# Optimization experiments

Measured on AMD Instinct MI355X. Metric: run time of the kernel, lower is better.

The kernel has to match this reference:

```python
import jax, jax.numpy as jnp
import numpy as np

H = 128          # hidden_channels
L = 2            # num_layers
E = 400000       # edges per relation
N_ATOM = 600000
N = (20000, 20000, 10000)  # node counts: 0=Chemical, 1=Gene, 2=Assay
OUT = 2          # out_channels
# (src_type, dst_type) per relation, matching the HeteroConv_att dict order
RELS = ((0,2),(0,2),(0,1),(0,1),(0,1),(2,1),(1,1),(2,0),(2,0),(1,0),(1,0),(1,0),(1,2))
R = len(RELS)
NEG_SLOPE = 0.2  # GATv2 LeakyReLU slope


def setup_inputs() -> dict:
    key = jax.random.key(0)
    ks = jax.random.split(key, 16)
    sc = 1.0 / np.sqrt(H)
    x_atom  = jax.random.normal(ks[0], (N_ATOM, H), jnp.float32)
    x_chem  = jax.random.normal(ks[1], (N[0], H), jnp.float32)
    x_gene  = jax.random.normal(ks[2], (N[1], H), jnp.float32)
    x_assay = jax.random.normal(ks[3], (N[2], H), jnp.float32)
    hyper_dst = jax.random.randint(ks[4], (N_ATOM,), 0, N[0], jnp.int32)
    ei = []
    for r, (s, d) in enumerate(RELS):
        src = jax.random.randint(jax.random.fold_in(ks[5], 2 * r), (E,), 0, N[s], jnp.int32)
        dst = jax.random.randint(jax.random.fold_in(ks[5], 2 * r + 1), (E,), 0, N[d], jnp.int32)
        ei.append(jnp.stack([src, dst]))
    edge_index_rel = jnp.stack(ei)  # [R, 2, E]
    W_mol = jax.random.normal(ks[6], (H, H), jnp.float32) * sc
    Wl    = jax.random.normal(ks[7], (L, R, H, H), jnp.float32) * sc
    Wr    = jax.random.normal(ks[8], (L, R, H, H), jnp.float32) * sc
    bl    = jnp.zeros((L, R, H), jnp.float32)
    br    = jnp.zeros((L, R, H), jnp.float32)
    att_a = jax.random.normal(ks[9], (L, R, H), jnp.float32) * sc
    cb    = jnp.zeros((L, R, H), jnp.float32)  # GATv2 output bias
    ln_g  = jnp.ones((L, 3, H), jnp.float32)   # LayerNorm gamma per (layer, node type)
    ln_b  = jnp.zeros((L, 3, H), jnp.float32)
    Wp    = jax.random.normal(ks[10], (H, OUT), jnp.float32) * sc
    bp    = jnp.zeros((OUT,), jnp.float32)
    return dict(x_atom=x_atom, x_chem=x_chem, x_gene=x_gene, x_assay=x_assay,
                W_mol=W_mol, Wl=Wl, Wr=Wr, bl=bl, br=br, att_a=att_a, cb=cb,
                ln_g=ln_g, ln_b=ln_b, Wp=Wp, bp=bp,
                hyper_dst=hyper_dst, edge_index_rel=edge_index_rel,
                chemical_label_task=0)


def _gatv2(x_src, x_dst, src, dst, Wl, Wr, bl, br, a, cb, n_dst):
    # GATv2Conv, single head, add_self_loops=False, share_weights=False
    xl = x_src @ Wl + bl                              # [Ns, H]
    xr = x_dst @ Wr + br                              # [Nd, H]
    e = jax.nn.leaky_relu(xl[src] + xr[dst], NEG_SLOPE) @ a  # [E]
    m = jax.ops.segment_max(e, dst, num_segments=n_dst)      # per-dst max
    ex = jnp.exp(e - m[dst])
    denom = jax.ops.segment_sum(ex, dst, num_segments=n_dst)
    alpha = ex / jnp.maximum(denom[dst], 1e-16)
    out = jax.ops.segment_sum(alpha[:, None] * xl[src], dst, num_segments=n_dst)
    return out + cb


def _layernorm(x, g, b):
    mu = x.mean(-1, keepdims=True)
    v = ((x - mu) ** 2).mean(-1, keepdims=True)
    return (x - mu) / jnp.sqrt(v + 1e-5) * g + b


def reference(x_atom, x_chem, x_gene, x_assay, W_mol, Wl, Wr, bl, br, att_a, cb,
              ln_g, ln_b, Wp, bp, hyper_dst, edge_index_rel, chemical_label_task):
    # molecular encoder (modeled as a linear projection over atom features)
    atom_enc = x_atom @ W_mol
    # bottom_up: mean-aggregate Atom -> Chemical, then add dst (Chemical) features
    ones = jnp.ones((N_ATOM,), atom_enc.dtype)
    cnt = jax.ops.segment_sum(ones, hyper_dst, num_segments=N[0])
    mean_agg = jax.ops.segment_sum(atom_enc, hyper_dst, num_segments=N[0]) \
               / jnp.maximum(cnt, 1.0)[:, None]
    xs = [mean_agg + x_chem, x_gene, x_assay]  # Chemical, Gene, Assay
    for l in range(L):
        agg = [jnp.zeros((N[t], H), x_chem.dtype) for t in range(3)]
        for r, (s, d) in enumerate(RELS):
            src = edge_index_rel[r, 0]
            dst = edge_index_rel[r, 1]
            out = _gatv2(xs[s], xs[d], src, dst, Wl[l, r], Wr[l, r], bl[l, r],
                         br[l, r], att_a[l, r], cb[l, r], N[d])
            agg[d] = agg[d] + out  # aggr='sum' across relations per dst type
        xs = [jax.nn.relu(_layernorm(agg[t], ln_g[l, t], ln_b[l, t])) for t in range(3)]
    return xs[0] @ Wp + bp  # pred_layer on Chemical nodes -> [N_chem, OUT]
```

## Files before the change

### kernel.cpp

```cpp
#include <hip/hip_runtime.h>
#include <math.h>

#define H 128
#define NLAYER 2
#define EDG 400000
#define NATOM 600000
#define NREL 13
#define SEGS 14
#define RDX 256
#define TILE 4096

typedef unsigned short u16;
typedef unsigned int u32;
using short8  = __attribute__((ext_vector_type(8))) short;
using ushort8 = __attribute__((ext_vector_type(8))) unsigned short;
using floatx4 = __attribute__((ext_vector_type(4))) float;

static constexpr int NODE_N[3]   = {20000, 20000, 10000};
static constexpr int TYPE_OFF[3] = {0, 20000, 40000};
static constexpr int SRC_T[NREL] = {0,0,0,0,0,2,1,2,2,1,1,1,1};
static constexpr int DST_T[NREL] = {2,2,1,1,1,1,1,0,0,0,0,0,2};

static constexpr int NREL_OF[3]    = {5, 5, 3};
static constexpr int RELS_OF[3][5] = {{7,8,9,10,11},{2,3,4,5,6},{0,1,12}};

static constexpr int XOFF_S[NREL] = {0,20000,40000,60000,80000,100000,110000,130000,140000,150000,170000,190000,210000};
static constexpr int XOFF_D[NREL] = {0,10000,20000,40000,60000,80000,100000,120000,140000,160000,180000,200000,220000};
#define XTOT 230000

static constexpr int SEG_N[SEGS]  = {20000,10000,10000,20000,20000,20000,20000,20000,20000,20000,20000,20000,20000,10000};
static constexpr int SEG_RO[SEGS] = {0,20001,30002,40003,60004,80005,100006,120007,140008,160009,180010,200011,220012,240013};
#define RP_TOTAL 250016

static constexpr int    SLEN[SEGS]   = {600000,EDG,EDG,EDG,EDG,EDG,EDG,EDG,EDG,EDG,EDG,EDG,EDG,EDG};
static constexpr int    RNB[SEGS]    = {147,98,98,98,98,98,98,98,98,98,98,98,98,98};
static constexpr int    RBHOFF[SEGS] = {0,37632,62720,87808,112896,137984,163072,188160,213248,238336,263424,288512,313600,338688};
#define BH_TOTAL 363776

__device__ __forceinline__ float wave_reduce_sum(float v) {
#pragma unroll
  for (int off = 32; off > 0; off >>= 1) v += __shfl_xor(v, off, 64);
  return v;
}

__device__ __forceinline__ u16 f2bf(float f) {
  union { float f; u32 u; } c; c.f = f;
  u32 u = c.u + 0x7fffu + ((c.u >> 16) & 1u);
  return (u16)(u >> 16);
}
__device__ __forceinline__ float bf2f(u16 h) { union { u32 i; float f; } c; c.i = (u32)h << 16; return c.f; }
__device__ __forceinline__ float bflo(u32 u) { union { u32 i; float f; } c; c.i = u << 16; return c.f; }
__device__ __forceinline__ float bfhi(u32 u) { union { u32 i; float f; } c; c.i = u & 0xffff0000u; return c.f; }

__device__ __forceinline__ int digof(u32 v, int shift) { return (int)((v >> shift) & 255u); }
__device__ __forceinline__ int digof(int2 v, int shift) { return (v.x >> shift) & 255; }


__global__ __launch_bounds__(256) void radix_init_a(const int* __restrict__ hyper, int2* __restrict__ Aa) {
  int i = blockIdx.x * 256 + threadIdx.x;
  if (i >= NATOM) return;
  Aa[i] = make_int2(hyper[i], i);
}

__global__ __launch_bounds__(256) void radix_init_e(const int* __restrict__ ei, u32* __restrict__ Ae) {
  int r = blockIdx.y;
  int i = blockIdx.x * 256 + threadIdx.x;
  if (i >= EDG) return;
  u32 src = (u32)ei[(size_t)(r * 2) * EDG + i];
  u32 dst = (u32)ei[(size_t)(r * 2 + 1) * EDG + i];
  Ae[(size_t)r * EDG + i] = (dst << 15) | src;
}

template <typename T>
__global__ __launch_bounds__(256) void radix_count_t(const T* __restrict__ in,
                                                     int* __restrict__ bh, int shift, int seg0) {
  int s = seg0 + blockIdx.y, bx = blockIdx.x;
  int nb = RNB[s];
  __shared__ int h[RDX];
  int t = threadIdx.x;
  h[t] = 0;
  __syncthreads();
  int len = SLEN[s];
  size_t poff = (s == 0) ? 0 : (size_t)(s - 1) * EDG;
#pragma unroll
  for (int i = 0; i < 16; ++i) {
    int p = bx * TILE + i * 256 + t;
    if (p < len) atomicAdd(&h[digof(in[poff + p], shift)], 1);
  }
  __syncthreads();
  bh[RBHOFF[s] + t * nb + bx] = h[t];
}

__global__ __launch_bounds__(256) void radix_scan(int* __restrict__ bh) {
  int s = blockIdx.x;
  int total = RNB[s] * RDX;
  int off = RBHOFF[s];
  __shared__ int sums[256];
  int t = threadIdx.x;
  int chunk = (total + 255) >> 8;
  int b = t * chunk, e = min(b + chunk, total);
  int acc = 0;
  for (int i = b; i < e; ++i) acc += bh[off + i];
  sums[t] = acc;
  __syncthreads();
  for (int o2 = 1; o2 < 256; o2 <<= 1) {
    int v = (t >= o2) ? sums[t - o2] : 0;
    __syncthreads();
    sums[t] += v;
    __syncthreads();
  }
  int pre = t ? sums[t - 1] : 0;
  for (int i = b; i < e; ++i) { int c = bh[off + i]; bh[off + i] = pre; pre += c; }
}

template <typename T>
__global__ __launch_bounds__(256) void radix_scat_t(const T* __restrict__ in,
                                                    T* __restrict__ out,
                                                    const int* __restrict__ bh, int shift, int seg0) {
  int s = seg0 + blockIdx.y, bx = blockIdx.x;
  int nb = RNB[s];
  __shared__ T stg[TILE];
  __shared__ int wc[4][RDX];
  __shared__ int pw[4][RDX];
  __shared__ int basev[RDX];
  __shared__ int lstart[RDX];
  __shared__ int delta[RDX];
  int t = threadIdx.x;
  int lane = t & 63, w = t >> 6;
  unsigned long long lmask = (1ull << lane) - 1ull;
  int len = SLEN[s];
  size_t poff = (s == 0) ? 0 : (size_t)(s - 1) * EDG;
  T kv[16]; int dg[16]; int rk[16];
  basev[t] = 0;
#pragma unroll
  for (int i = 0; i < 16; ++i) {
    int p = bx * TILE + i * 256 + t;
    kv[i] = (p < len) ? in[poff + p] : T{};
  }
  __syncthreads();
  for (int i = 0; i < 16; ++i) {
    int p = bx * TILE + i * 256 + t;
    bool valid = p < len;
    int d = digof(kv[i], shift);
    wc[0][t] = 0; wc[1][t] = 0; wc[2][t] = 0; wc[3][t] = 0;
    __syncthreads();
    unsigned long long m = __ballot(valid);
#pragma unroll
    for (int b2 = 0; b2 < 8; ++b2) {
      unsigned long long bal = __ballot((d >> b2) & 1);
      m &= ((d >> b2) & 1) ? bal : ~bal;
    }
    int riw = __popcll(m & lmask);
    if (valid && riw == 0) wc[w][d] = __popcll(m);
    __syncthreads();
    int s0 = 0;
#pragma unroll
    for (int ww = 0; ww < 4; ++ww) { pw[ww][t] = s0; s0 += wc[ww][t]; }
    __syncthreads();
    dg[i] = d;
    rk[i] = basev[d] + pw[w][d] + riw;
    __syncthreads();
    basev[t] += s0;
    __syncthreads();
  }
  int tot = basev[t];
  pw[0][t] = tot;
  __syncthreads();
  for (int o2 = 1; o2 < 256; o2 <<= 1) {
    int v = (t >= o2) ? pw[0][t - o2] : 0;
    __syncthreads();
    pw[0][t] += v;
    __syncthreads();
  }
  int ls = pw[0][t] - tot;
  lstart[t] = ls;
  delta[t] = bh[RBHOFF[s] + t * nb + bx] - ls;
  __syncthreads();
#pragma unroll
  for (int i = 0; i < 16; ++i) {
    int p = bx * TILE + i * 256 + t;
    if (p < len) stg[lstart[dg[i]] + rk[i]] = kv[i];
  }
  __syncthreads();
  int vc = min(len - bx * TILE, TILE);
#pragma unroll
  for (int i = 0; i < 16; ++i) {
    int p = i * 256 + t;
    if (p < vc) {
      T pr = stg[p];
      int d = digof(pr, shift);
      out[poff + delta[d] + p] = pr;
    }
  }
}

__global__ __launch_bounds__(256) void build_rp_a(const int2* __restrict__ Aa, int* __restrict__ rp) {
  int j = blockIdx.x * 256 + threadIdx.x;
  if (j >= NATOM) return;
  int k = Aa[j].x;
  int kprev = (j == 0) ? -1 : Aa[j - 1].x;
  for (int d = kprev + 1; d <= k; ++d) rp[d] = j;
  if (j == NATOM - 1)
    for (int d = k + 1; d <= 20000; ++d) rp[d] = NATOM;
}

__global__ __launch_bounds__(256) void build_rp_e(const u32* __restrict__ Ae, int* __restrict__ rp) {
  int r = blockIdx.y;
  int j = blockIdx.x * 256 + threadIdx.x;
  if (j >= EDG) return;
  const u32* Ar = Ae + (size_t)r * EDG;
  int ro = SEG_RO[r + 1];
  int n = SEG_N[r + 1];
  int k = (int)(Ar[j] >> 15);
  int kprev = (j == 0) ? -1 : (int)(Ar[j - 1] >> 15);
  for (int d = kprev + 1; d <= k; ++d) rp[ro + d] = j;
  if (j == EDG - 1)
    for (int d = k + 1; d <= n; ++d) rp[ro + d] = EDG;
}


__global__ __launch_bounds__(256) void mean_atoms(const float* __restrict__ x_atom,
                                                  const int* __restrict__ rp,
                                                  const int2* __restrict__ pairs,
                                                  float* __restrict__ Mean) {
  int wave = (blockIdx.x * blockDim.x + threadIdx.x) >> 6;
  int lane = threadIdx.x & 63;
  int g = lane >> 5, l32 = lane & 31;
  int chem = wave * 2 + g;
  if (chem >= 20000) return;
  int b = rp[chem], e = rp[chem + 1];
  float4 s = make_float4(0.f, 0.f, 0.f, 0.f);
  for (int j = b; j < e; ++j) {
    int a = pairs[j].y;
    float4 v = *(const float4*)(x_atom + (size_t)a * H + l32 * 4);
    s.x += v.x; s.y += v.y; s.z += v.z; s.w += v.w;
  }
  float inv = 1.0f / fmaxf((float)(e - b), 1.0f);
  float4 o; o.x = s.x * inv; o.y = s.y * inv; o.z = s.z * inv; o.w = s.w * inv;
  *(float4*)(Mean + (size_t)chem * H + l32 * 4) = o;
}


__global__ __launch_bounds__(256) void proj_kernel(
    const float* __restrict__ X, const float* __restrict__ W,
    const float* __restrict__ Res, u16* __restrict__ Yb, int N) {
  int r0 = blockIdx.x * 64;
  if (r0 >= N) return;
  __shared__ float Xs[64][132];
  int tid = threadIdx.x;
#pragma unroll
  for (int i = 0; i < 8; ++i) {
    int f = tid + 256 * i;
    int row = f >> 5, c4 = (f & 31) << 2;
    float4 v = make_float4(0.f, 0.f, 0.f, 0.f);
    if (r0 + row < N) v = *(const float4*)(X + (size_t)(r0 + row) * H + c4);
    *(float4*)&Xs[row][c4] = v;
  }
  __syncthreads();
  int trow = tid >> 5, tcol = tid & 31;
  float acc[8][4] = {};
#pragma unroll 4
  for (int k = 0; k < 128; ++k) {
    float4 w = *(const float4*)(W + k * H + tcol * 4);
#pragma unroll
    for (int i = 0; i < 8; ++i) {
      float xv = Xs[trow * 8 + i][k];
      acc[i][0] = fmaf(xv, w.x, acc[i][0]);
      acc[i][1] = fmaf(xv, w.y, acc[i][1]);
      acc[i][2] = fmaf(xv, w.z, acc[i][2]);
      acc[i][3] = fmaf(xv, w.w, acc[i][3]);
    }
  }
#pragma unroll
  for (int i = 0; i < 8; ++i) {
    int row = r0 + trow * 8 + i;
    if (row < N) {
      float4 rv = *(const float4*)(Res + (size_t)row * H + tcol * 4);
      u32 lo = (u32)f2bf(acc[i][0] + rv.x) | ((u32)f2bf(acc[i][1] + rv.y) << 16);
      u32 hi = (u32)f2bf(acc[i][2] + rv.z) | ((u32)f2bf(acc[i][3] + rv.w) << 16);
      *(uint2*)(Yb + (size_t)row * H + tcol * 4) = make_uint2(lo, hi);
    }
  }
}


__global__ __launch_bounds__(256) void conv_xs(const float* __restrict__ x_gene,
                                               const float* __restrict__ x_assay,
                                               u16* __restrict__ xsb) {
  int idx = 20000 * H + (blockIdx.x * 256 + threadIdx.x) * 4;
  if (idx >= 50000 * H) return;
  int row = idx >> 7;
  const float* src = (row < 40000) ? x_gene + (idx - 20000 * H) : x_assay + (idx - 40000 * H);
  float4 v = *(const float4*)src;
  u32 p0 = (u32)f2bf(v.x) | ((u32)f2bf(v.y) << 16);
  u32 p1 = (u32)f2bf(v.z) | ((u32)f2bf(v.w) << 16);
  u32* o = (u32*)(xsb + idx);
  o[0] = p0; o[1] = p1;
}

__global__ __launch_bounds__(256) void conv_weights(const float* __restrict__ Wl,
                                                    const float* __restrict__ Wr,
                                                    u16* __restrict__ WB) {
  int mat = blockIdx.x;
  int side = blockIdx.y;
  const float* W = (side ? Wr : Wl) + (size_t)mat * H * H;
  u16* O = WB + ((size_t)mat * 2 + side) * H * H;
  for (int f = threadIdx.x; f < H * H; f += 256) {
    int n = f >> 7, k = f & 127;
    O[f] = f2bf(W[k * H + n]);
  }
}


__global__ __launch_bounds__(256) void proj_mfma(
    const u16* __restrict__ xsb, const u16* __restrict__ WB,
    const float* __restrict__ bl, const float* __restrict__ br,
    u16* __restrict__ XLb, u16* __restrict__ XRb, int layer) {
  int by = blockIdx.y;
  int r = by >> 1, side = by & 1;
  int typ = side ? DST_T[r] : SRC_T[r];
  int N = NODE_N[typ];
  int r0 = blockIdx.x * 64;
  if (r0 >= N) return;
  const u16* X = xsb + (size_t)TYPE_OFF[typ] * H;
  const u16* W = WB + ((size_t)(layer * NREL + r) * 2 + side) * H * H;
  const float* bias = (side ? br : bl) + (size_t)(layer * NREL + r) * H;
  u16* Y = side ? (XRb + (size_t)XOFF_D[r] * H) : (XLb + (size_t)XOFF_S[r] * H);

  __shared__ u16 Xs[64 * 136];
  __shared__ u16 Ws[128 * 136];
  int tid = threadIdx.x;
#pragma unroll
  for (int i = 0; i < 4; ++i) {
    int f = tid + 256 * i;
    int row = f >> 4, seg = f & 15;
    ushort8 v = {};
    if (r0 + row < N) v = *(const ushort8*)(X + (size_t)(r0 + row) * H + seg * 8);
    *(ushort8*)(Xs + row * 136 + seg * 8) = v;
  }
#pragma unroll
  for (int i = 0; i < 8; ++i) {
    int f = tid + 256 * i;
    int row = f >> 4, seg = f & 15;
    *(ushort8*)(Ws + row * 136 + seg * 8) = *(const ushort8*)(W + row * H + seg * 8);
  }
  __syncthreads();

  int w = tid >> 6, lane = tid & 63;
  int g = lane >> 4, l16 = lane & 15;
  floatx4 acc[4][2] = {};
#pragma unroll
  for (int kt = 0; kt < 4; ++kt) {
    int k0 = kt * 32 + g * 8;
    short8 a[4], b[2];
#pragma unroll
    for (int rt = 0; rt < 4; ++rt) a[rt] = *(const short8*)(Xs + (rt * 16 + l16) * 136 + k0);
#pragma unroll
    for (int ct = 0; ct < 2; ++ct) b[ct] = *(const short8*)(Ws + (w * 32 + ct * 16 + l16) * 136 + k0);
#pragma unroll
    for (int rt = 0; rt < 4; ++rt)
#pragma unroll
      for (int ct = 0; ct < 2; ++ct)
        acc[rt][ct] = __builtin_amdgcn_mfma_f32_16x16x32_bf16(a[rt], b[ct], acc[rt][ct], 0, 0, 0);
  }
  __syncthreads();
  float bv0 = bias[w * 32 + l16];
  float bv1 = bias[w * 32 + 16 + l16];
#pragma unroll
  for (int rt = 0; rt < 4; ++rt)
#pragma unroll
    for (int ct = 0; ct < 2; ++ct) {
      float bv = ct ? bv1 : bv0;
      int col = w * 32 + ct * 16 + l16;
#pragma unroll
      for (int reg = 0; reg < 4; ++reg) {
        int row = rt * 16 + g * 4 + reg;
        Xs[row * 136 + col] = f2bf(acc[rt][ct][reg] + bv);
      }
    }
  __syncthreads();
#pragma unroll
  for (int i = 0; i < 4; ++i) {
    int f = tid + 256 * i;
    int row = f >> 4, seg = f & 15;
    if (r0 + row < N)
      *(ushort8*)(Y + (size_t)(r0 + row) * H + seg * 8) = *(const ushort8*)(Xs + row * 136 + seg * 8);
  }
}


__global__ __launch_bounds__(256) void gat_fused(
    const u16* __restrict__ XLb, const u16* __restrict__ XRb,
    const int* __restrict__ rp, const u32* __restrict__ Ae,
    const float* __restrict__ att_a, const float* __restrict__ cbv,
    float* __restrict__ agg, int layer) {
  int wave = (blockIdx.x * blockDim.x + threadIdx.x) >> 6;
  int lane = threadIdx.x & 63;
  int g = lane >> 4, l16 = lane & 15;
  int d = wave * 4 + g;
  bool dv = d < 50000;
  int dd = dv ? d : 49999;
  int dt = dd < 20000 ? 0 : (dd < 40000 ? 1 : 2);
  int dl = dd - TYPE_OFF[dt];
  float o[8] = {};
  int nr = NREL_OF[dt];
  for (int rr = 0; rr < nr; ++rr) {
    int r = RELS_OF[dt][rr];
    size_t wi = (size_t)layer * NREL + r;
    const u16* XL = XLb + (size_t)XOFF_S[r] * H;
    ushort8 uxr = *(const ushort8*)(XRb + (size_t)(XOFF_D[r] + dl) * H + l16 * 8);
    float4 a0 = *(const float4*)(att_a + wi * H + l16 * 8);
    float4 a1 = *(const float4*)(att_a + wi * H + l16 * 8 + 4);
    float av[8] = {a0.x, a0.y, a0.z, a0.w, a1.x, a1.y, a1.z, a1.w};
    float xr[8];
#pragma unroll
    for (int c = 0; c < 8; ++c) xr[c] = bf2f((u16)uxr[c]);
    const int* rpr = rp + SEG_RO[r + 1];
    const u32* pe = Ae + (size_t)r * EDG;
    int b = dv ? rpr[dl] : 0;
    int e = dv ? rpr[dl + 1] : 0;
    float m = -1e30f, s = 0.f;
    float V[8] = {};
    int j = b;
    if ((e - b) & 1) {
      int src = (int)(pe[j] & 32767u);
      ushort8 u0 = *(const ushort8*)(XL + (size_t)src * H + l16 * 8);
      float t = 0.f;
#pragma unroll
      for (int c = 0; c < 8; ++c) {
        V[c] = bf2f((u16)u0[c]);
        float v = V[c] + xr[c];
        t = fmaf(av[c], fmaxf(v, 0.2f * v), t);
      }
      t += __shfl_xor(t, 1, 64); t += __shfl_xor(t, 2, 64);
      t += __shfl_xor(t, 4, 64); t += __shfl_xor(t, 8, 64);
      s = 1.0f;
      m = t;
      ++j;
    }
    for (; j < e; j += 2) {
      u32 p0 = pe[j], p1 = pe[j + 1];
      int s0 = (int)(p0 & 32767u), s1 = (int)(p1 & 32767u);
      ushort8 u0 = *(const ushort8*)(XL + (size_t)s0 * H + l16 * 8);
      ushort8 u1 = *(const ushort8*)(XL + (size_t)s1 * H + l16 * 8);
      float xl0[8], xl1[8], t0 = 0.f, t1 = 0.f;
#pragma unroll
      for (int c = 0; c < 8; ++c) {
        xl0[c] = bf2f((u16)u0[c]);
        xl1[c] = bf2f((u16)u1[c]);
        float v0 = xl0[c] + xr[c], v1 = xl1[c] + xr[c];
        t0 = fmaf(av[c], fmaxf(v0, 0.2f * v0), t0);
        t1 = fmaf(av[c], fmaxf(v1, 0.2f * v1), t1);
      }
      t0 += __shfl_xor(t0, 1, 64); t1 += __shfl_xor(t1, 1, 64);
      t0 += __shfl_xor(t0, 2, 64); t1 += __shfl_xor(t1, 2, 64);
      t0 += __shfl_xor(t0, 4, 64); t1 += __shfl_xor(t1, 4, 64);
      t0 += __shfl_xor(t0, 8, 64); t1 += __shfl_xor(t1, 8, 64);
      float nm = fmaxf(m, fmaxf(t0, t1));
      float sc = __expf(m - nm);
      float w0 = __expf(t0 - nm), w1 = __expf(t1 - nm);
      s = fmaf(s, sc, w0 + w1);
#pragma unroll
      for (int c = 0; c < 8; ++c)
        V[c] = fmaf(V[c], sc, fmaf(w0, xl0[c], w1 * xl1[c]));
      m = nm;
    }
    if (s > 0.f) {
      float inv = 1.0f / s;
#pragma unroll
      for (int c = 0; c < 8; ++c) o[c] = fmaf(V[c], inv, o[c]);
    }
    float4 c0 = *(const float4*)(cbv + wi * H + l16 * 8);
    float4 c1 = *(const float4*)(cbv + wi * H + l16 * 8 + 4);
    o[0] += c0.x; o[1] += c0.y; o[2] += c0.z; o[3] += c0.w;
    o[4] += c1.x; o[5] += c1.y; o[6] += c1.z; o[7] += c1.w;
  }
  if (dv) {
    float* ap = agg + (size_t)dd * H + l16 * 8;
    *(float4*)ap       = make_float4(o[0], o[1], o[2], o[3]);
    *(float4*)(ap + 4) = make_float4(o[4], o[5], o[6], o[7]);
  }
}


__global__ __launch_bounds__(256) void ln_relu_kernel(const float* __restrict__ agg,
                                                      const float* __restrict__ g,
                                                      const float* __restrict__ b,
                                                      u16* __restrict__ xsb) {
  int row = (blockIdx.x * blockDim.x + threadIdx.x) >> 6;
  int lane = threadIdx.x & 63;
  if (row >= 50000) return;
  int t = row < 20000 ? 0 : (row < 40000 ? 1 : 2);
  float2 x = *(const float2*)(agg + (size_t)row * H + 2 * lane);
  float mu = wave_reduce_sum(x.x + x.y) * (1.f / 128.f);
  float d0 = x.x - mu, d1 = x.y - mu;
  float var = wave_reduce_sum(d0 * d0 + d1 * d1) * (1.f / 128.f);
  float inv = 1.0f / sqrtf(var + 1e-5f);
  float2 gg = *(const float2*)(g + t * H + 2 * lane);
  float2 bb = *(const float2*)(b + t * H + 2 * lane);
  float o0 = fmaxf(d0 * inv * gg.x + bb.x, 0.f);
  float o1 = fmaxf(d1 * inv * gg.y + bb.y, 0.f);
  u32 pk = (u32)f2bf(o0) | ((u32)f2bf(o1) << 16);
  *(u32*)(xsb + (size_t)row * H + 2 * lane) = pk;
}


__global__ __launch_bounds__(256) void pred_kernel(const u16* __restrict__ xsb,
                                                   const float* __restrict__ Wp,
                                                   const float* __restrict__ bp,
                                                   float* __restrict__ out) {
  int row = (blockIdx.x * blockDim.x + threadIdx.x) >> 6;
  int lane = threadIdx.x & 63;
  if (row >= 20000) return;
  u32 u = *(const u32*)(xsb + (size_t)row * H + 2 * lane);
  float x0 = bflo(u), x1 = bfhi(u);
  float4 w = *(const float4*)(Wp + 4 * lane);
  float pA = x0 * w.x + x1 * w.z;
  float pB = x0 * w.y + x1 * w.w;
  pA = wave_reduce_sum(pA);
  pB = wave_reduce_sum(pB);
  if (lane == 0) {
    out[(size_t)row * 2 + 0] = pA + bp[0];
    out[(size_t)row * 2 + 1] = pB + bp[1];
  }
}


extern "C" void kernel_launch(void* const* d_in, const int* in_sizes, int n_in,
                              void* d_out, int out_size, void* d_ws, size_t ws_size,
                              hipStream_t stream) {
  (void)in_sizes; (void)n_in; (void)out_size; (void)ws_size;
  const float* x_atom  = (const float*)d_in[0];
  const float* x_chem  = (const float*)d_in[1];
  const float* x_gene  = (const float*)d_in[2];
  const float* x_assay = (const float*)d_in[3];
  const float* W_mol   = (const float*)d_in[4];
  const float* Wl      = (const float*)d_in[5];
  const float* Wr      = (const float*)d_in[6];
  const float* bl      = (const float*)d_in[7];
  const float* br      = (const float*)d_in[8];
  const float* att_a   = (const float*)d_in[9];
  const float* cb      = (const float*)d_in[10];
  const float* ln_g    = (const float*)d_in[11];
  const float* ln_b    = (const float*)d_in[12];
  const float* Wp      = (const float*)d_in[13];
  const float* bp      = (const float*)d_in[14];
  const int*   hyper   = (const int*)d_in[15];
  const int*   ei      = (const int*)d_in[16];
  float* out = (float*)d_out;

  float* ws = (float*)d_ws;
  size_t o = 0;
  float* agg  = ws + o; o += (size_t)50000 * H;
  float* Mean = ws + o; o += (size_t)20000 * H;
  int2*  Aa   = (int2*)(ws + o); o += (size_t)2 * NATOM;
  int2*  Ba   = (int2*)(ws + o); o += (size_t)2 * NATOM;
  u32*   Ae   = (u32*)(ws + o); o += (size_t)NREL * EDG;
  u32*   Be   = (u32*)(ws + o); o += (size_t)NREL * EDG;
  int*   rp   = (int*)(ws + o); o += RP_TOTAL;
  int*   bh   = (int*)(ws + o); o += BH_TOTAL;
  u16*   xsb  = (u16*)(ws + o); o += (size_t)50000 * H / 2;
  u16*   WB   = (u16*)(ws + o); o += (size_t)52 * H * H / 2;
  u16*   XLb  = (u16*)(ws + o); o += (size_t)XTOT * H / 2;
  u16*   XRb  = (u16*)(ws + o); o += (size_t)XTOT * H / 2;

  dim3 b256(256);

  radix_init_a<<<dim3(2344), b256, 0, stream>>>(hyper, Aa);
  radix_init_e<<<dim3(1563, 13), b256, 0, stream>>>(ei, Ae);
  radix_count_t<int2><<<dim3(147, 1), b256, 0, stream>>>(Aa, bh, 0, 0);
  radix_count_t<u32><<<dim3(98, 13), b256, 0, stream>>>(Ae, bh, 15, 1);
  radix_scan<<<SEGS, b256, 0, stream>>>(bh);
  radix_scat_t<int2><<<dim3(147, 1), b256, 0, stream>>>(Aa, Ba, bh, 0, 0);
  radix_scat_t<u32><<<dim3(98, 13), b256, 0, stream>>>(Ae, Be, bh, 15, 1);
  radix_count_t<int2><<<dim3(147, 1), b256, 0, stream>>>(Ba, bh, 8, 0);
  radix_count_t<u32><<<dim3(98, 13), b256, 0, stream>>>(Be, bh, 23, 1);
  radix_scan<<<SEGS, b256, 0, stream>>>(bh);
  radix_scat_t<int2><<<dim3(147, 1), b256, 0, stream>>>(Ba, Aa, bh, 8, 0);
  radix_scat_t<u32><<<dim3(98, 13), b256, 0, stream>>>(Be, Ae, bh, 23, 1);
  build_rp_a<<<dim3(2344), b256, 0, stream>>>(Aa, rp);
  build_rp_e<<<dim3(1563, 13), b256, 0, stream>>>(Ae, rp);

  mean_atoms<<<dim3(20000 / 8), b256, 0, stream>>>(x_atom, rp, Aa, Mean);
  proj_kernel<<<dim3(313), b256, 0, stream>>>(Mean, W_mol, x_chem, xsb, 20000);
  conv_xs<<<dim3(3750), b256, 0, stream>>>(x_gene, x_assay, xsb);
  conv_weights<<<dim3(26, 2), b256, 0, stream>>>(Wl, Wr, WB);

  for (int l = 0; l < NLAYER; ++l) {
    proj_mfma<<<dim3(313, 26), b256, 0, stream>>>(xsb, WB, bl, br, XLb, XRb, l);
    gat_fused<<<dim3(3125), b256, 0, stream>>>(XLb, XRb, rp, Ae, att_a, cb, agg, l);
    ln_relu_kernel<<<dim3(50000 / 4), b256, 0, stream>>>(agg, ln_g + l * 3 * H, ln_b + l * 3 * H, xsb);
  }
  pred_kernel<<<dim3(20000 / 4), b256, 0, stream>>>(xsb, Wp, bp, out);
}
```

Measured before the change: 1.475 ms.

## Merge per-relation CSR into single per-destination edge list with degree-sorted scheduling

```diff
diff --git a/kernel.cpp b/kernel.cpp
--- a/kernel.cpp
+++ b/kernel.cpp
@@ -23,6 +23,7 @@
 
 static constexpr int NREL_OF[3]    = {5, 5, 3};
 static constexpr int RELS_OF[3][5] = {{7,8,9,10,11},{2,3,4,5,6},{0,1,12}};
+static constexpr int RR_LOCAL[NREL] = {0,1,0,1,2,3,4,0,1,2,3,4,2};
 
 static constexpr int XOFF_S[NREL] = {0,20000,40000,60000,80000,100000,110000,130000,140000,150000,170000,190000,210000};
 static constexpr int XOFF_D[NREL] = {0,10000,20000,40000,60000,80000,100000,120000,140000,160000,180000,200000,220000};
@@ -219,6 +220,111 @@
 }
 
 
+__global__ __launch_bounds__(256) void merged_meta(const int* __restrict__ rp,
+                                                   int* __restrict__ pre,
+                                                   int* __restrict__ deg) {
+  int d = blockIdx.x * 256 + threadIdx.x;
+  if (d >= 50000) return;
+  int dt = d < 20000 ? 0 : (d < 40000 ? 1 : 2);
+  int dl = d - TYPE_OFF[dt];
+  int nr = NREL_OF[dt];
+  int acc = 0;
+  for (int rr = 0; rr < nr; ++rr) {
+    int r = RELS_OF[dt][rr];
+    const int* rpr = rp + SEG_RO[r + 1];
+    pre[XOFF_D[r] + dl] = acc;
+    acc += rpr[dl + 1] - rpr[dl];
+  }
+  deg[d] = acc;
+}
+
+__global__ __launch_bounds__(256) void scan_deg(const int* __restrict__ deg, int* __restrict__ rpm) {
+  __shared__ int sums[256];
+  int t = threadIdx.x;
+  const int chunk = 196;
+  int b = t * chunk, e = min(b + chunk, 50000);
+  int acc = 0;
+  for (int i = b; i < e; ++i) acc += deg[i];
+  sums[t] = acc;
+  __syncthreads();
+  for (int o2 = 1; o2 < 256; o2 <<= 1) {
+    int v = (t >= o2) ? sums[t - o2] : 0;
+    __syncthreads();
+    sums[t] += v;
+    __syncthreads();
+  }
+  int pre = t ? sums[t - 1] : 0;
+  for (int i = b; i < e; ++i) { rpm[i] = pre; pre += deg[i]; }
+  if (t == 255) rpm[50000] = pre;
+}
+
+__global__ __launch_bounds__(256) void build_perm(const int* __restrict__ deg, int* __restrict__ perm) {
+  int ty = blockIdx.x;
+  int tid = threadIdx.x;
+  __shared__ int hist[1024];
+  __shared__ int ws2[256];
+  int n = NODE_N[ty], off = TYPE_OFF[ty];
+  for (int i = tid; i < 1024; i += 256) hist[i] = 0;
+  __syncthreads();
+  for (int i = tid; i < n; i += 256) {
+    int k = 1023 - min(deg[off + i], 1023);
+    atomicAdd(&hist[k], 1);
+  }
+  __syncthreads();
+  int s0 = 0;
+#pragma unroll
+  for (int q = 0; q < 4; ++q) s0 += hist[tid * 4 + q];
+  ws2[tid] = s0;
+  __syncthreads();
+  for (int o2 = 1; o2 < 256; o2 <<= 1) {
+    int v = (tid >= o2) ? ws2[tid - o2] : 0;
+    __syncthreads();
+    ws2[tid] += v;
+    __syncthreads();
+  }
+  int pre2 = tid ? ws2[tid - 1] : 0;
+  int vals[4];
+#pragma unroll
+  for (int q = 0; q < 4; ++q) { vals[q] = pre2; pre2 += hist[tid * 4 + q]; }
+  __syncthreads();
+#pragma unroll
+  for (int q = 0; q < 4; ++q) hist[tid * 4 + q] = vals[q];
+  __syncthreads();
+  for (int i = tid; i < n; i += 256) {
+    int k = 1023 - min(deg[off + i], 1023);
+    int pos = atomicAdd(&hist[k], 1);
+    perm[off + pos] = off + i;
+  }
+}
+
+__global__ __launch_bounds__(256) void merged_scatter(const u32* __restrict__ Ae,
+                                                      const int* __restrict__ rp,
+                                                      const int* __restrict__ rpm,
+                                                      const int* __restrict__ pre,
+                                                      u32* __restrict__ Em) {
+  int r = blockIdx.y;
+  int j = blockIdx.x * 256 + threadIdx.x;
+  if (j >= EDG) return;
+  u32 p = Ae[(size_t)r * EDG + j];
+  int dst = (int)(p >> 15);
+  int src = (int)(p & 32767u);
+  int dt = DST_T[r];
+  int rank = j - rp[SEG_RO[r + 1] + dst];
+  int pos = rpm[TYPE_OFF[dt] + dst] + pre[XOFF_D[r] + dst] + rank;
+  Em[pos] = ((u32)RR_LOCAL[r] << 18) | (u32)(XOFF_S[r] + src);
+}
+
+__global__ __launch_bounds__(256) void cb_sum(const float* __restrict__ cb, float* __restrict__ cbs) {
+  int i = blockIdx.x * 256 + threadIdx.x;
+  if (i >= NLAYER * 3 * H) return;
+  int c = i & 127, t = (i >> 7) % 3, l = i / (3 * H);
+  float s = 0.f;
+  for (int rr = 0; rr < NREL_OF[t]; ++rr)
+    s += cb[((size_t)l * NREL + RELS_OF[t][rr]) * H + c];
+  cbs[i] = s;
+}
+
+
 __global__ __launch_bounds__(256) void mean_atoms(const float* __restrict__ x_atom,
                                                   const int* __restrict__ rp,
                                                   const int2* __restrict__ pairs,
@@ -391,59 +497,55 @@
 
 __global__ __launch_bounds__(256) void gat_fused(
     const u16* __restrict__ XLb, const u16* __restrict__ XRb,
-    const int* __restrict__ rp, const u32* __restrict__ Ae,
-    const float* __restrict__ att_a, const float* __restrict__ cbv,
-    float* __restrict__ agg, int layer) {
+    const int* __restrict__ rpm, const u32* __restrict__ Em,
+    const float* __restrict__ att_a, const float* __restrict__ cbs,
+    const int* __restrict__ perm, float* __restrict__ agg, int layer) {
   int wave = (blockIdx.x * blockDim.x + threadIdx.x) >> 6;
   int lane = threadIdx.x & 63;
   int g = lane >> 4, l16 = lane & 15;
-  int d = wave * 4 + g;
-  bool dv = d < 50000;
-  int dd = dv ? d : 49999;
-  int dt = dd < 20000 ? 0 : (dd < 40000 ? 1 : 2);
-  int dl = dd - TYPE_OFF[dt];
+  int idx = wave * 4 + g;
+  if (idx >= 50000) return;
+  int dt = idx < 20000 ? 0 : (idx < 40000 ? 1 : 2);
+  int d = perm[idx];
+  int dl = d - TYPE_OFF[dt];
+  int b = rpm[d], e = rpm[d + 1];
   float o[8] = {};
-  int nr = NREL_OF[dt];
-  for (int rr = 0; rr < nr; ++rr) {
-    int r = RELS_OF[dt][rr];
-    size_t wi = (size_t)layer * NREL + r;
-    const u16* XL = XLb + (size_t)XOFF_S[r] * H;
-    ushort8 uxr = *(const ushort8*)(XRb + (size_t)(XOFF_D[r] + dl) * H + l16 * 8);
-    float4 a0 = *(const float4*)(att_a + wi * H + l16 * 8);
-    float4 a1 = *(const float4*)(att_a + wi * H + l16 * 8 + 4);
-    float av[8] = {a0.x, a0.y, a0.z, a0.w, a1.x, a1.y, a1.z, a1.w};
-    float xr[8];
-#pragma unroll
-    for (int c = 0; c < 8; ++c) xr[c] = bf2f((u16)uxr[c]);
-    const int* rpr = rp + SEG_RO[r + 1];
-    const u32* pe = Ae + (size_t)r * EDG;
-    int b = dv ? rpr[dl] : 0;
-    int e = dv ? rpr[dl + 1] : 0;
-    float m = -1e30f, s = 0.f;
-    float V[8] = {};
-    int j = b;
-    if ((e - b) & 1) {
-      int src = (int)(pe[j] & 32767u);
-      ushort8 u0 = *(const ushort8*)(XL + (size_t)src * H + l16 * 8);
-      float t = 0.f;
-#pragma unroll
-      for (int c = 0; c < 8; ++c) {
-        V[c] = bf2f((u16)u0[c]);
-        float v = V[c] + xr[c];
-        t = fmaf(av[c], fmaxf(v, 0.2f * v), t);
+  float V[8] = {}, xr[8] = {}, av[8] = {};
+  float m = -1e30f, s = 0.f;
+  int cur = -1;
+  int j = b;
+  while (j < e) {
+    u32 p0 = Em[j];
+    int rr0 = (int)(p0 >> 18);
+    if (rr0 != cur) {
+      if (cur >= 0) {
+        float inv = 1.0f / s;
+#pragma unroll
+        for (int c = 0; c < 8; ++c) o[c] = fmaf(V[c], inv, o[c]);
       }
-      t += __shfl_xor(t, 1, 64); t += __shfl_xor(t, 2, 64);
-      t += __shfl_xor(t, 4, 64); t += __shfl_xor(t, 8, 64);
-      s = 1.0f;
-      m = t;
-      ++j;
+      m = -1e30f; s = 0.f;
+#pragma unroll
+      for (int c = 0; c < 8; ++c) V[c] = 0.f;
+      cur = rr0;
+      int r = RELS_OF[dt][rr0];
+      size_t wi = (size_t)layer * NREL + r;
+      ushort8 uxr = *(const ushort8*)(XRb + ((size_t)(XOFF_D[r] + dl) << 7) + (l16 << 3));
+      float4 a0 = *(const float4*)(att_a + wi * H + (l16 << 3));
+      float4 a1 = *(const float4*)(att_a + wi * H + (l16 << 3) + 4);
+      av[0] = a0.x; av[1] = a0.y; av[2] = a0.z; av[3] = a0.w;
+      av[4] = a1.x; av[5] = a1.y; av[6] = a1.z; av[7] = a1.w;
+#pragma unroll
+      for (int c = 0; c < 8; ++c) xr[c] = bf2f((u16)uxr[c]);
     }
-    for (; j < e; j += 2) {
-      u32 p0 = pe[j], p1 = pe[j + 1];
-      int s0 = (int)(p0 & 32767u), s1 = (int)(p1 & 32767u);
-      ushort8 u0 = *(const ushort8*)(XL + (size_t)s0 * H + l16 * 8);
-      ushort8 u1 = *(const ushort8*)(XL + (size_t)s1 * H + l16 * 8);
-      float xl0[8], xl1[8], t0 = 0.f, t1 = 0.f;
+    bool two = false;
+    u32 p1 = 0;
+    if (j + 1 < e) { p1 = Em[j + 1]; two = ((int)(p1 >> 18) == cur); }
+    if (two) {
+      int row0 = (int)(p0 & 0x3ffffu), row1 = (int)(p1 & 0x3ffffu);
+      ushort8 u0 = *(const ushort8*)(XLb + ((size_t)row0 << 7) + (l16 << 3));
+      ushort8 u1 = *(const ushort8*)(XLb + ((size_t)row1 << 7) + (l16 << 3));
+      float xl0[8], xl1[8];
+      float t0 = 0.f, t1 = 0.f;
 #pragma unroll
       for (int c = 0; c < 8; ++c) {
         xl0[c] = bf2f((u16)u0[c]);
@@ -464,22 +566,45 @@
       for (int c = 0; c < 8; ++c)
         V[c] = fmaf(V[c], sc, fmaf(w0, xl0[c], w1 * xl1[c]));
       m = nm;
+      j += 2;
+    } else {
+      int row0 = (int)(p0 & 0x3ffffu);
+      ushort8 u0 = *(const ushort8*)(XLb + ((size_t)row0 << 7) + (l16 << 3));
+      float xl0[8];
+      float t0 = 0.f;
+#pragma unroll
+      for (int c = 0; c < 8; ++c) {
+        xl0[c] = bf2f((u16)u0[c]);
+        float v0 = xl0[c] + xr[c];
+        t0 = fmaf(av[c], fmaxf(v0, 0.2f * v0), t0);
+      }
+      t0 += __shfl_xor(t0, 1, 64);
+      t0 += __shfl_xor(t0, 2, 64);
+      t0 += __shfl_xor(t0, 4, 64);
+      t0 += __shfl_xor(t0, 8, 64);
+      float nm = fmaxf(m, t0);
+      float sc = __expf(m - nm);
+      float w0 = __expf(t0 - nm);
+      s = fmaf(s, sc, w0);
+#pragma unroll
+      for (int c = 0; c < 8; ++c) V[c] = fmaf(V[c], sc, w0 * xl0[c]);
+      m = nm;
+      ++j;
     }
-    if (s > 0.f) {
-      float inv = 1.0f / s;
-#pragma unroll
-      for (int c = 0; c < 8; ++c) o[c] = fmaf(V[c], inv, o[c]);
-    }
-    float4 c0 = *(const float4*)(cbv + wi * H + l16 * 8);
-    float4 c1 = *(const float4*)(cbv + wi * H + l16 * 8 + 4);
-    o[0] += c0.x; o[1] += c0.y; o[2] += c0.z; o[3] += c0.w;
-    o[4] += c1.x; o[5] += c1.y; o[6] += c1.z; o[7] += c1.w;
-  }
-  if (dv) {
-    float* ap = agg + (size_t)dd * H + l16 * 8;
-    *(float4*)ap       = make_float4(o[0], o[1], o[2], o[3]);
-    *(float4*)(ap + 4) = make_float4(o[4], o[5], o[6], o[7]);
-  }
+  }
+  if (cur >= 0) {
+    float inv = 1.0f / s;
+#pragma unroll
+    for (int c = 0; c < 8; ++c) o[c] = fmaf(V[c], inv, o[c]);
+  }
+  const float* cp = cbs + ((size_t)layer * 3 + dt) * H + (l16 << 3);
+  float4 c0 = *(const float4*)cp;
+  float4 c1 = *(const float4*)(cp + 4);
+  o[0] += c0.x; o[1] += c0.y; o[2] += c0.z; o[3] += c0.w;
+  o[4] += c1.x; o[5] += c1.y; o[6] += c1.z; o[7] += c1.w;
+  float* ap = agg + (size_t)d * H + (l16 << 3);
+  *(float4*)ap       = make_float4(o[0], o[1], o[2], o[3]);
+  *(float4*)(ap + 4) = make_float4(o[4], o[5], o[6], o[7]);
 }
 
 
@@ -563,6 +688,12 @@
   u16*   WB   = (u16*)(ws + o); o += (size_t)52 * H * H / 2;
   u16*   XLb  = (u16*)(ws + o); o += (size_t)XTOT * H / 2;
   u16*   XRb  = (u16*)(ws + o); o += (size_t)XTOT * H / 2;
+  int*   rpm  = (int*)(ws + o); o += 50004;
+  int*   pre  = (int*)(ws + o); o += 230000;
+  int*   deg  = (int*)(ws + o); o += 50000;
+  int*   perm = (int*)(ws + o); o += 50000;
+  float* cbs  = ws + o; o += (size_t)NLAYER * 3 * H;
+  u32*   Em   = Be;
 
   dim3 b256(256);
 
@@ -581,6 +712,12 @@
   build_rp_a<<<dim3(2344), b256, 0, stream>>>(Aa, rp);
   build_rp_e<<<dim3(1563, 13), b256, 0, stream>>>(Ae, rp);
 
+  merged_meta<<<dim3(196), b256, 0, stream>>>(rp, pre, deg);
+  scan_deg<<<dim3(1), b256, 0, stream>>>(deg, rpm);
+  build_perm<<<dim3(3), b256, 0, stream>>>(deg, perm);
+  merged_scatter<<<dim3(1563, 13), b256, 0, stream>>>(Ae, rp, rpm, pre, Em);
+  cb_sum<<<dim3(3), b256, 0, stream>>>(cb, cbs);
+
   mean_atoms<<<dim3(20000 / 8), b256, 0, stream>>>(x_atom, rp, Aa, Mean);
   proj_kernel<<<dim3(313), b256, 0, stream>>>(Mean, W_mol, x_chem, xsb, 20000);
   conv_xs<<<dim3(3750), b256, 0, stream>>>(x_gene, x_assay, xsb);
@@ -588,7 +725,7 @@
 
   for (int l = 0; l < NLAYER; ++l) {
     proj_mfma<<<dim3(313, 26), b256, 0, stream>>>(xsb, WB, bl, br, XLb, XRb, l);
-    gat_fused<<<dim3(3125), b256, 0, stream>>>(XLb, XRb, rp, Ae, att_a, cb, agg, l);
+    gat_fused<<<dim3(3125), b256, 0, stream>>>(XLb, XRb, rpm, Em, att_a, cbs, perm, agg, l);
     ln_relu_kernel<<<dim3(50000 / 4), b256, 0, stream>>>(agg, ln_g + l * 3 * H, ln_b + l * 3 * H, xsb);
   }
   pred_kernel<<<dim3(20000 / 4), b256, 0, stream>>>(xsb, Wp, bp, out);
```

After: 1.707 ms. 1.16x slower.

## Software-pipeline edge gathers in GAT kernel and drop online-softmax max tracking

Applied to the files above, without the earlier changes.

```diff
diff --git a/kernel.cpp b/kernel.cpp
--- a/kernel.cpp
+++ b/kernel.cpp
@@ -389,7 +389,7 @@
 }
 
 
-__global__ __launch_bounds__(256) void gat_fused(
+__global__ __launch_bounds__(256, 8) void gat_fused(
     const u16* __restrict__ XLb, const u16* __restrict__ XRb,
     const int* __restrict__ rp, const u32* __restrict__ Ae,
     const float* __restrict__ att_a, const float* __restrict__ cbv,
@@ -398,51 +398,28 @@
   int lane = threadIdx.x & 63;
   int g = lane >> 4, l16 = lane & 15;
   int d = wave * 4 + g;
-  bool dv = d < 50000;
-  int dd = dv ? d : 49999;
-  int dt = dd < 20000 ? 0 : (dd < 40000 ? 1 : 2);
-  int dl = dd - TYPE_OFF[dt];
+  int dt = d < 20000 ? 0 : (d < 40000 ? 1 : 2);
+  int dl = d - TYPE_OFF[dt];
   float o[8] = {};
   int nr = NREL_OF[dt];
   for (int rr = 0; rr < nr; ++rr) {
     int r = RELS_OF[dt][rr];
     size_t wi = (size_t)layer * NREL + r;
-    const u16* XL = XLb + (size_t)XOFF_S[r] * H;
-    ushort8 uxr = *(const ushort8*)(XRb + (size_t)(XOFF_D[r] + dl) * H + l16 * 8);
-    float4 a0 = *(const float4*)(att_a + wi * H + l16 * 8);
-    float4 a1 = *(const float4*)(att_a + wi * H + l16 * 8 + 4);
+    const u16* XL = XLb + ((size_t)XOFF_S[r] << 7);
+    ushort8 uxr = *(const ushort8*)(XRb + ((size_t)(XOFF_D[r] + dl) << 7) + (l16 << 3));
+    float4 a0 = *(const float4*)(att_a + wi * H + (l16 << 3));
+    float4 a1 = *(const float4*)(att_a + wi * H + (l16 << 3) + 4);
     float av[8] = {a0.x, a0.y, a0.z, a0.w, a1.x, a1.y, a1.z, a1.w};
     float xr[8];
 #pragma unroll
     for (int c = 0; c < 8; ++c) xr[c] = bf2f((u16)uxr[c]);
     const int* rpr = rp + SEG_RO[r + 1];
     const u32* pe = Ae + (size_t)r * EDG;
-    int b = dv ? rpr[dl] : 0;
-    int e = dv ? rpr[dl + 1] : 0;
-    float m = -1e30f, s = 0.f;
+    int b = rpr[dl], e = rpr[dl + 1];
+    float s = 0.f;
     float V[8] = {};
-    int j = b;
-    if ((e - b) & 1) {
-      int src = (int)(pe[j] & 32767u);
-      ushort8 u0 = *(const ushort8*)(XL + (size_t)src * H + l16 * 8);
-      float t = 0.f;
-#pragma unroll
-      for (int c = 0; c < 8; ++c) {
-        V[c] = bf2f((u16)u0[c]);
-        float v = V[c] + xr[c];
-        t = fmaf(av[c], fmaxf(v, 0.2f * v), t);
-      }
-      t += __shfl_xor(t, 1, 64); t += __shfl_xor(t, 2, 64);
-      t += __shfl_xor(t, 4, 64); t += __shfl_xor(t, 8, 64);
-      s = 1.0f;
-      m = t;
-      ++j;
-    }
-    for (; j < e; j += 2) {
-      u32 p0 = pe[j], p1 = pe[j + 1];
-      int s0 = (int)(p0 & 32767u), s1 = (int)(p1 & 32767u);
-      ushort8 u0 = *(const ushort8*)(XL + (size_t)s0 * H + l16 * 8);
-      ushort8 u1 = *(const ushort8*)(XL + (size_t)s1 * H + l16 * 8);
+
+    auto pair_acc = [&](const ushort8& u0, const ushort8& u1) {
       float xl0[8], xl1[8], t0 = 0.f, t1 = 0.f;
 #pragma unroll
       for (int c = 0; c < 8; ++c) {
@@ -456,30 +433,63 @@
       t0 += __shfl_xor(t0, 2, 64); t1 += __shfl_xor(t1, 2, 64);
       t0 += __shfl_xor(t0, 4, 64); t1 += __shfl_xor(t1, 4, 64);
       t0 += __shfl_xor(t0, 8, 64); t1 += __shfl_xor(t1, 8, 64);
-      float nm = fmaxf(m, fmaxf(t0, t1));
-      float sc = __expf(m - nm);
-      float w0 = __expf(t0 - nm), w1 = __expf(t1 - nm);
-      s = fmaf(s, sc, w0 + w1);
+      float w0 = __expf(t0), w1 = __expf(t1);
+      s += w0 + w1;
 #pragma unroll
       for (int c = 0; c < 8; ++c)
-        V[c] = fmaf(V[c], sc, fmaf(w0, xl0[c], w1 * xl1[c]));
-      m = nm;
+        V[c] = fmaf(w1, xl1[c], fmaf(w0, xl0[c], V[c]));
+    };
+
+    int npair = (e - b) >> 1;
+    int j = b;
+    if (npair > 0) {
+      u32 i0 = pe[j], i1 = pe[j + 1];
+      u32 i2 = pe[j + 2], i3 = pe[j + 3];
+      ushort8 u0 = *(const ushort8*)(XL + ((size_t)(i0 & 32767u) << 7) + (l16 << 3));
+      ushort8 u1 = *(const ushort8*)(XL + ((size_t)(i1 & 32767u) << 7) + (l16 << 3));
+      for (int it = 1; it < npair; ++it) {
+        ushort8 n0 = *(const ushort8*)(XL + ((size_t)(i2 & 32767u) << 7) + (l16 << 3));
+        ushort8 n1 = *(const ushort8*)(XL + ((size_t)(i3 & 32767u) << 7) + (l16 << 3));
+        i2 = pe[j + 2 * it + 2];
+        i3 = pe[j + 2 * it + 3];
+        pair_acc(u0, u1);
+        u0 = n0; u1 = n1;
+      }
+      pair_acc(u0, u1);
+      j += 2 * npair;
+    }
+    if (j < e) {
+      u32 p0 = pe[j];
+      ushort8 u0 = *(const ushort8*)(XL + ((size_t)(p0 & 32767u) << 7) + (l16 << 3));
+      float xl0[8], t0 = 0.f;
+#pragma unroll
+      for (int c = 0; c < 8; ++c) {
+        xl0[c] = bf2f((u16)u0[c]);
+        float v0 = xl0[c] + xr[c];
+        t0 = fmaf(av[c], fmaxf(v0, 0.2f * v0), t0);
+      }
+      t0 += __shfl_xor(t0, 1, 64);
+      t0 += __shfl_xor(t0, 2, 64);
+      t0 += __shfl_xor(t0, 4, 64);
+      t0 += __shfl_xor(t0, 8, 64);
+      float w0 = __expf(t0);
+      s += w0;
+#pragma unroll
+      for (int c = 0; c < 8; ++c) V[c] = fmaf(w0, xl0[c], V[c]);
     }
     if (s > 0.f) {
       float inv = 1.0f / s;
 #pragma unroll
       for (int c = 0; c < 8; ++c) o[c] = fmaf(V[c], inv, o[c]);
     }
-    float4 c0 = *(const float4*)(cbv + wi * H + l16 * 8);
-    float4 c1 = *(const float4*)(cbv + wi * H + l16 * 8 + 4);
+    float4 c0 = *(const float4*)(cbv + wi * H + (l16 << 3));
+    float4 c1 = *(const float4*)(cbv + wi * H + (l16 << 3) + 4);
     o[0] += c0.x; o[1] += c0.y; o[2] += c0.z; o[3] += c0.w;
     o[4] += c1.x; o[5] += c1.y; o[6] += c1.z; o[7] += c1.w;
   }
-  if (dv) {
-    float* ap = agg + (size_t)dd * H + l16 * 8;
-    *(float4*)ap       = make_float4(o[0], o[1], o[2], o[3]);
-    *(float4*)(ap + 4) = make_float4(o[4], o[5], o[6], o[7]);
-  }
+  float* ap = agg + ((size_t)d << 7) + (l16 << 3);
+  *(float4*)ap       = make_float4(o[0], o[1], o[2], o[3]);
+  *(float4*)(ap + 4) = make_float4(o[4], o[5], o[6], o[7]);
 }
 
 
```

After: 1.660 ms. +12.5%, slower.
